# Performance work log

Hardware: AMD Instinct MI355X
Metric: run time of the kernel (lower is better)

## Reference

```python
import jax, jax.numpy as jnp
import jax.scipy.linalg as jsl
import numpy as np

EPS = 1e-6          # config.eps
MIN_EIG = 1e-4      # config.min_eigenvalue
B, N, K = 2, 2048, 3


def _so3_generators():
    # standard so(3) basis: [G_c]_{kl} = -eps_{ckl}
    G = np.zeros((3, 3, 3), np.float32)
    G[0, 1, 2] = -1.0; G[0, 2, 1] = 1.0
    G[1, 0, 2] = 1.0;  G[1, 2, 0] = -1.0
    G[2, 0, 1] = -1.0; G[2, 1, 0] = 1.0
    return jnp.asarray(G)


def _spd(key, b, n, k):
    # well-conditioned SPD covariances (as a real model would produce)
    A = jax.random.normal(key, (b, n, k, k), jnp.float32)
    return jnp.einsum('bnkl,bnml->bnkm', A, A) / k + 0.5 * jnp.eye(k, dtype=jnp.float32)


def setup_inputs() -> dict:
    key = jax.random.key(0)
    k0, k1, k2, k3 = jax.random.split(key, 4)
    Sigma_prior = _spd(k0, B, N, K)
    Sigma_q = _spd(k1, B, N, K)
    phi = jax.random.normal(k2, (B, N, K), jnp.float32)          # gauge field, C == K == 3
    beta = jax.random.uniform(k3, (B, N, N), jnp.float32) / N    # attention-like weights, rows O(1)
    return {
        'Sigma_prior': Sigma_prior,
        'Sigma_q': Sigma_q,
        'phi': phi,
        'beta': beta,
        'generators': _so3_generators(),
    }


def _batched_expm(mats):
    # mats: (B, N, K, K) -> elementwise matrix exponential
    b, n, k, _ = mats.shape
    return jax.vmap(jsl.expm)(mats.reshape(-1, k, k)).reshape(b, n, k, k)


def reference(Sigma_prior, Sigma_q, phi, beta, generators):
    b, n, k, _ = Sigma_prior.shape
    I = jnp.eye(k, dtype=Sigma_prior.dtype)

    # precisions (regularized inverses)
    Lambda_p = jnp.linalg.inv(Sigma_prior + EPS * I)   # (B,N,K,K)
    Lambda_q = jnp.linalg.inv(Sigma_q + EPS * I)       # (B,N,K,K)

    # gauge transport Omega_ij = e^{phi_i} e^{-phi_j}
    phi_mat = jnp.einsum('bnc,ckl->bnkl', phi, generators)
    exp_phi = _batched_expm(phi_mat)
    exp_neg_phi = _batched_expm(-phi_mat)
    Omega = jnp.einsum('bikl,bjlm->bijkm', exp_phi, exp_neg_phi)   # (B,N,N,K,K)

    # transported neighbor precision: Omega Lambda_q Omega^T
    Lt = jnp.einsum('bijkl,bjlm,bijnm->bijkn', Omega, Lambda_q, Omega)

    # incoming social term: sum_j beta_ij * Lt_ij
    M_in = jnp.einsum('bij,bijkl->bikl', beta, Lt)

    # outgoing recoil: (sum_j beta_ji) * Lambda_q_i
    M_out = beta.sum(axis=1)[..., None, None] * Lambda_q

    M = Lambda_p + M_in + M_out
    M = 0.5 * (M + jnp.swapaxes(M, -1, -2))

    # eigenvalue floor + inverse via eigh
    w, V = jnp.linalg.eigh(M)
    w = jnp.maximum(w, MIN_EIG)
    M_pd = jnp.einsum('bnkl,bnl,bnml->bnkm', V, w, V)
    M_inv = jnp.einsum('bnkl,bnl,bnml->bnkm', V, 1.0 / w, V)
    return M_pd, M_inv
```

## Files before the change

kernel.cpp:

```cpp
#include <hip/hip_runtime.h>
#include <math.h>

#define EPS_REG 1e-6f
#define MIN_EIG_F 1e-4f
#define RB 8
#define NCH2 32


__device__ __forceinline__ void sym_inv3(const float m[3][3], float o[3][3]) {
    float c00 = m[1][1]*m[2][2] - m[1][2]*m[2][1];
    float c01 = m[1][2]*m[2][0] - m[1][0]*m[2][2];
    float c02 = m[1][0]*m[2][1] - m[1][1]*m[2][0];
    float det = m[0][0]*c00 + m[0][1]*c01 + m[0][2]*c02;
    float inv = 1.0f / det;
    o[0][0] = c00*inv;
    o[1][0] = c01*inv;
    o[2][0] = c02*inv;
    o[0][1] = (m[0][2]*m[2][1]-m[0][1]*m[2][2])*inv;
    o[1][1] = (m[0][0]*m[2][2]-m[0][2]*m[2][0])*inv;
    o[2][1] = (m[0][1]*m[2][0]-m[0][0]*m[2][1])*inv;
    o[0][2] = (m[0][1]*m[1][2]-m[0][2]*m[1][1])*inv;
    o[1][2] = (m[0][2]*m[1][0]-m[0][0]*m[1][2])*inv;
    o[2][2] = (m[0][0]*m[1][1]-m[0][1]*m[1][0])*inv;
}

__device__ __forceinline__ void jrot(float A[3][3], float V[3][3], int p, int q) {
    float apq = A[p][q];
    if (fabsf(apq) < 1e-20f) return;
    float theta = (A[q][q] - A[p][p]) / (2.0f * apq);
    float t = 1.0f / (fabsf(theta) + sqrtf(1.0f + theta*theta));
    if (theta < 0.0f) t = -t;
    float c = 1.0f / sqrtf(1.0f + t*t);
    float s = t * c;
    int r = 3 - p - q;
    float apq_t = t*apq;
    A[p][p] -= apq_t;
    A[q][q] += apq_t;
    A[p][q] = 0.0f; A[q][p] = 0.0f;
    float arp = A[r][p], arq = A[r][q];
    A[r][p] = c*arp - s*arq; A[p][r] = A[r][p];
    A[r][q] = s*arp + c*arq; A[q][r] = A[r][q];
    #pragma unroll
    for (int k = 0; k < 3; k++) {
        float vkp = V[k][p], vkq = V[k][q];
        V[k][p] = c*vkp - s*vkq;
        V[k][q] = s*vkp + c*vkq;
    }
}

__global__ void precompute_kernel(const float* __restrict__ Sp,
                                  const float* __restrict__ Sq,
                                  const float* __restrict__ phi,
                                  float* __restrict__ Lp,
                                  float* __restrict__ Lq,
                                  float* __restrict__ Rm,
                                  float* __restrict__ S,
                                  int BN) {
    int t = blockIdx.x * blockDim.x + threadIdx.x;
    if (t >= BN) return;

    float m[3][3], lq[3][3], lp[3][3];
    const float* p = Sq + (size_t)t * 9;
    #pragma unroll
    for (int i = 0; i < 3; i++)
        #pragma unroll
        for (int j = 0; j < 3; j++) m[i][j] = p[i*3 + j];
    m[0][0] += EPS_REG; m[1][1] += EPS_REG; m[2][2] += EPS_REG;
    sym_inv3(m, lq);

    p = Sp + (size_t)t * 9;
    #pragma unroll
    for (int i = 0; i < 3; i++)
        #pragma unroll
        for (int j = 0; j < 3; j++) m[i][j] = p[i*3 + j];
    m[0][0] += EPS_REG; m[1][1] += EPS_REG; m[2][2] += EPS_REG;
    sym_inv3(m, lp);

    float* o = Lq + (size_t)t * 6;
    o[0]=lq[0][0]; o[1]=lq[0][1]; o[2]=lq[0][2]; o[3]=lq[1][1]; o[4]=lq[1][2]; o[5]=lq[2][2];
    o = Lp + (size_t)t * 6;
    o[0]=lp[0][0]; o[1]=lp[0][1]; o[2]=lp[0][2]; o[3]=lp[1][1]; o[4]=lp[1][2]; o[5]=lp[2][2];

    float w0 = phi[(size_t)t*3], w1 = phi[(size_t)t*3+1], w2 = phi[(size_t)t*3+2];
    float th2 = w0*w0 + w1*w1 + w2*w2;
    float th = sqrtf(th2);
    float a, b;
    if (th < 1e-4f) { a = 1.0f - th2*(1.0f/6.0f); b = 0.5f - th2*(1.0f/24.0f); }
    else            { a = sinf(th)/th;            b = (1.0f - cosf(th))/th2; }
    float R[3][3];
    R[0][0] = 1.0f + b*(w0*w0 - th2); R[0][1] = -a*w2 + b*w0*w1;        R[0][2] =  a*w1 + b*w0*w2;
    R[1][0] =  a*w2 + b*w0*w1;        R[1][1] = 1.0f + b*(w1*w1 - th2); R[1][2] = -a*w0 + b*w1*w2;
    R[2][0] = -a*w1 + b*w0*w2;        R[2][1] =  a*w0 + b*w1*w2;        R[2][2] = 1.0f + b*(w2*w2 - th2);
    o = Rm + (size_t)t * 9;
    #pragma unroll
    for (int i = 0; i < 3; i++)
        #pragma unroll
        for (int j = 0; j < 3; j++) o[i*3 + j] = R[i][j];

    float U[3][3], Sv[3][3];
    #pragma unroll
    for (int i = 0; i < 3; i++)
        #pragma unroll
        for (int j = 0; j < 3; j++)
            U[i][j] = lq[i][0]*R[0][j] + lq[i][1]*R[1][j] + lq[i][2]*R[2][j];
    #pragma unroll
    for (int i = 0; i < 3; i++)
        #pragma unroll
        for (int j = 0; j < 3; j++)
            Sv[i][j] = R[0][i]*U[0][j] + R[1][i]*U[1][j] + R[2][i]*U[2][j];
    o = S + (size_t)t * 6;
    o[0]=Sv[0][0]; o[1]=Sv[0][1]; o[2]=Sv[0][2]; o[3]=Sv[1][1]; o[4]=Sv[1][2]; o[5]=Sv[2][2];
}

__global__ __launch_bounds__(256) void fused_beta_kernel(
        const float* __restrict__ beta,
        const float* __restrict__ S,
        float* __restrict__ T,
        float* __restrict__ partial,
        int B, int N) {
    int tid = threadIdx.x;
    int grow0 = blockIdx.x * RB;
    int b = grow0 / N;
    int chunksPerB = N / RB;
    int chunk = (grow0 - b * N) / RB;
    const float* sb = S + (size_t)b * N * 6;

    float acc[RB][6];
    #pragma unroll
    for (int r = 0; r < RB; r++)
        #pragma unroll
        for (int c = 0; c < 6; c++) acc[r][c] = 0.0f;

    int jtiles = N / 1024;
    for (int jt = 0; jt < jtiles; jt++) {
        int c0 = jt * 1024 + 4 * tid;
        float4 s4[6];
        const float4* sp = (const float4*)(sb + (size_t)c0 * 6);
        #pragma unroll
        for (int u = 0; u < 6; u++) s4[u] = sp[u];
        const float* sv = (const float*)s4;

        float csum0 = 0.f, csum1 = 0.f, csum2 = 0.f, csum3 = 0.f;
        #pragma unroll
        for (int r = 0; r < RB; r++) {
            float4 w4 = *(const float4*)(beta + (size_t)(grow0 + r) * N + c0);
            csum0 += w4.x; csum1 += w4.y; csum2 += w4.z; csum3 += w4.w;
            #pragma unroll
            for (int c = 0; c < 6; c++) {
                acc[r][c] += w4.x * sv[0*6 + c];
                acc[r][c] += w4.y * sv[1*6 + c];
                acc[r][c] += w4.z * sv[2*6 + c];
                acc[r][c] += w4.w * sv[3*6 + c];
            }
        }
        *(float4*)(partial + ((size_t)b * chunksPerB + chunk) * N + c0) =
            make_float4(csum0, csum1, csum2, csum3);
    }

    __shared__ float red[256][49];
    __shared__ float red2[4][48];
    #pragma unroll
    for (int r = 0; r < RB; r++)
        #pragma unroll
        for (int c = 0; c < 6; c++)
            red[tid][r * 6 + c] = acc[r][c];
    __syncthreads();
    if (tid < 192) {
        int v = tid % 48, grp = tid / 48;
        float s = 0.0f;
        #pragma unroll 8
        for (int r = 0; r < 64; r++) s += red[grp * 64 + r][v];
        red2[grp][v] = s;
    }
    __syncthreads();
    if (tid < 48) {
        float v = red2[0][tid] + red2[1][tid] + red2[2][tid] + red2[3][tid];
        T[(size_t)grow0 * 6 + tid] = v;
    }
}

__global__ void colsum_hop_kernel(const float* __restrict__ partial,
                                  float* __restrict__ partial2,
                                  int B, int N) {
    int colTiles = N / 256;
    int idx = blockIdx.x;
    int ct  = idx % colTiles;
    int g   = (idx / colTiles) % NCH2;
    int b   = idx / (colTiles * NCH2);
    int col = ct * 256 + threadIdx.x;
    int chunksPerB = N / RB;
    int chg = chunksPerB / NCH2;
    const float* p = partial + ((size_t)b * chunksPerB + g * chg) * N + col;
    float s = 0.0f;
    #pragma unroll 8
    for (int k = 0; k < chg; k++) { s += *p; p += N; }
    partial2[((size_t)b * NCH2 + g) * N + col] = s;
}

__global__ void finalize_kernel(const float* __restrict__ Lp,
                                const float* __restrict__ Lq,
                                const float* __restrict__ Rm,
                                const float* __restrict__ T,
                                const float* __restrict__ partial2,
                                float* __restrict__ out,
                                int B, int N) {
    int t = blockIdx.x * blockDim.x + threadIdx.x;
    int BN = B * N;
    if (t >= BN) return;
    int b = t / N;
    int i = t - b * N;

    float cs = 0.0f;
    #pragma unroll 8
    for (int c = 0; c < NCH2; c++)
        cs += partial2[((size_t)b * NCH2 + c) * N + i];

    const float* p = Rm + (size_t)t * 9;
    float R[3][3];
    #pragma unroll
    for (int ii = 0; ii < 3; ii++)
        #pragma unroll
        for (int jj = 0; jj < 3; jj++) R[ii][jj] = p[ii*3 + jj];

    const float* tp = T + (size_t)t * 6;
    float Tm[3][3] = {{tp[0],tp[1],tp[2]},{tp[1],tp[3],tp[4]},{tp[2],tp[4],tp[5]}};
    const float* lpp = Lp + (size_t)t * 6;
    const float* lqp = Lq + (size_t)t * 6;
    float Lpf[3][3] = {{lpp[0],lpp[1],lpp[2]},{lpp[1],lpp[3],lpp[4]},{lpp[2],lpp[4],lpp[5]}};
    float Lqf[3][3] = {{lqp[0],lqp[1],lqp[2]},{lqp[1],lqp[3],lqp[4]},{lqp[2],lqp[4],lqp[5]}};

    float U[3][3], M[3][3];
    #pragma unroll
    for (int ii = 0; ii < 3; ii++)
        #pragma unroll
        for (int jj = 0; jj < 3; jj++)
            U[ii][jj] = R[ii][0]*Tm[0][jj] + R[ii][1]*Tm[1][jj] + R[ii][2]*Tm[2][jj];
    #pragma unroll
    for (int ii = 0; ii < 3; ii++)
        #pragma unroll
        for (int jj = 0; jj < 3; jj++) {
            float min_ij = U[ii][0]*R[jj][0] + U[ii][1]*R[jj][1] + U[ii][2]*R[jj][2];
            M[ii][jj] = Lpf[ii][jj] + min_ij + cs * Lqf[ii][jj];
        }
    float A[3][3];
    #pragma unroll
    for (int ii = 0; ii < 3; ii++)
        #pragma unroll
        for (int jj = 0; jj < 3; jj++) A[ii][jj] = 0.5f * (M[ii][jj] + M[jj][ii]);

    float V[3][3] = {{1,0,0},{0,1,0},{0,0,1}};
    #pragma unroll
    for (int sweep = 0; sweep < 6; sweep++) {
        jrot(A, V, 0, 1);
        jrot(A, V, 0, 2);
        jrot(A, V, 1, 2);
    }
    float w0 = fmaxf(A[0][0], MIN_EIG_F);
    float w1 = fmaxf(A[1][1], MIN_EIG_F);
    float w2 = fmaxf(A[2][2], MIN_EIG_F);
    float iw0 = 1.0f/w0, iw1 = 1.0f/w1, iw2 = 1.0f/w2;

    float* opd = out + (size_t)t * 9;
    float* oin = out + (size_t)BN * 9 + (size_t)t * 9;
    #pragma unroll
    for (int ii = 0; ii < 3; ii++)
        #pragma unroll
        for (int jj = 0; jj < 3; jj++) {
            float pd = V[ii][0]*w0*V[jj][0] + V[ii][1]*w1*V[jj][1] + V[ii][2]*w2*V[jj][2];
            float iv = V[ii][0]*iw0*V[jj][0] + V[ii][1]*iw1*V[jj][1] + V[ii][2]*iw2*V[jj][2];
            opd[ii*3 + jj] = pd;
            oin[ii*3 + jj] = iv;
        }
}

extern "C" void kernel_launch(void* const* d_in, const int* in_sizes, int n_in,
                              void* d_out, int out_size, void* d_ws, size_t ws_size,
                              hipStream_t stream) {
    const float* Sp   = (const float*)d_in[0];
    const float* Sq   = (const float*)d_in[1];
    const float* phi  = (const float*)d_in[2];
    const float* beta = (const float*)d_in[3];

    int BN = in_sizes[2] / 3;
    int N  = (int)((long long)in_sizes[3] / BN);
    int B  = BN / N;

    float* ws = (float*)d_ws;
    float* Lp = ws;
    float* Lq = Lp + (size_t)BN * 6;
    float* Rm = Lq + (size_t)BN * 6;
    float* S  = Rm + (size_t)BN * 9;
    float* T  = S  + (size_t)BN * 6;
    float* partial  = T + (size_t)BN * 6;
    float* partial2 = partial + (size_t)BN / RB * N;

    float* outf = (float*)d_out;

    precompute_kernel<<<(BN + 63)/64, 64, 0, stream>>>(Sp, Sq, phi, Lp, Lq, Rm, S, BN);

    fused_beta_kernel<<<BN / RB, 256, 0, stream>>>(beta, S, T, partial, B, N);

    int colTiles = N / 256;
    colsum_hop_kernel<<<B * NCH2 * colTiles, 256, 0, stream>>>(partial, partial2, B, N);

    finalize_kernel<<<(BN + 63)/64, 64, 0, stream>>>(Lp, Lq, Rm, T, partial2, outf, B, N);
}
```

Measured before the change: 26.84 us.

## Fuse column-sum reduction into finalize and recompute precisions instead of storing

Removes the separate colsum_hop kernel. The finalize kernel now reduces the partial column sums directly with 4 sub-waves per 64 points. Lp, Lq and the rotation matrices are no longer written to workspace; finalize recomputes them from the raw inputs. Global loads and stores in the precompute and finalize kernels are staged through shared memory with coalesced float4 accesses. This saves one launch and intermediate traffic, at the cost of a longer serial column reduction per block and only 64 of 256 threads doing the math.

```diff
diff --git a/kernel.cpp b/kernel.cpp
--- a/kernel.cpp
+++ b/kernel.cpp
@@ -4,7 +4,6 @@
 #define EPS_REG 1e-6f
 #define MIN_EIG_F 1e-4f
 #define RB 8
-#define NCH2 32
 
 
 __device__ __forceinline__ void sym_inv3(const float m[3][3], float o[3][3]) {
@@ -22,6 +21,17 @@
     o[0][2] = (m[0][1]*m[1][2]-m[0][2]*m[1][1])*inv;
     o[1][2] = (m[0][2]*m[1][0]-m[0][0]*m[1][2])*inv;
     o[2][2] = (m[0][0]*m[1][1]-m[0][1]*m[1][0])*inv;
+}
+
+__device__ __forceinline__ void rodrigues(float w0, float w1, float w2, float R[3][3]) {
+    float th2 = w0*w0 + w1*w1 + w2*w2;
+    float th = sqrtf(th2);
+    float a, b;
+    if (th < 1e-4f) { a = 1.0f - th2*(1.0f/6.0f); b = 0.5f - th2*(1.0f/24.0f); }
+    else            { a = sinf(th)/th;            b = (1.0f - cosf(th))/th2; }
+    R[0][0] = 1.0f + b*(w0*w0 - th2); R[0][1] = -a*w2 + b*w0*w1;        R[0][2] =  a*w1 + b*w0*w2;
+    R[1][0] =  a*w2 + b*w0*w1;        R[1][1] = 1.0f + b*(w1*w1 - th2); R[1][2] = -a*w0 + b*w1*w2;
+    R[2][0] = -a*w1 + b*w0*w2;        R[2][1] =  a*w0 + b*w1*w2;        R[2][2] = 1.0f + b*(w2*w2 - th2);
 }
 
 __device__ __forceinline__ void jrot(float A[3][3], float V[3][3], int p, int q) {
@@ -48,68 +58,53 @@
     }
 }
 
-__global__ void precompute_kernel(const float* __restrict__ Sp,
-                                  const float* __restrict__ Sq,
-                                  const float* __restrict__ phi,
-                                  float* __restrict__ Lp,
-                                  float* __restrict__ Lq,
-                                  float* __restrict__ Rm,
-                                  float* __restrict__ S,
-                                  int BN) {
-    int t = blockIdx.x * blockDim.x + threadIdx.x;
-    if (t >= BN) return;
-
-    float m[3][3], lq[3][3], lp[3][3];
-    const float* p = Sq + (size_t)t * 9;
+__global__ __launch_bounds__(64) void precompute_S_kernel(
+        const float* __restrict__ Sq,
+        const float* __restrict__ phi,
+        float* __restrict__ S,
+        int BN) {
+    __shared__ float sq_s[576];
+    __shared__ float ph_s[192];
+    __shared__ float so_s[384];
+    int tid = threadIdx.x;
+    int p0 = blockIdx.x * 64;
+
+    const float4* src = (const float4*)(Sq + (size_t)p0 * 9);
+    #pragma unroll
+    for (int i = tid; i < 144; i += 64) ((float4*)sq_s)[i] = src[i];
+    const float4* psrc = (const float4*)(phi + (size_t)p0 * 3);
+    if (tid < 48) ((float4*)ph_s)[tid] = psrc[tid];
+    __syncthreads();
+
+    float m[3][3], lq[3][3];
     #pragma unroll
     for (int i = 0; i < 3; i++)
         #pragma unroll
-        for (int j = 0; j < 3; j++) m[i][j] = p[i*3 + j];
+        for (int j = 0; j < 3; j++) m[i][j] = sq_s[tid*9 + i*3 + j];
     m[0][0] += EPS_REG; m[1][1] += EPS_REG; m[2][2] += EPS_REG;
     sym_inv3(m, lq);
 
-    p = Sp + (size_t)t * 9;
-    #pragma unroll
-    for (int i = 0; i < 3; i++)
-        #pragma unroll
-        for (int j = 0; j < 3; j++) m[i][j] = p[i*3 + j];
-    m[0][0] += EPS_REG; m[1][1] += EPS_REG; m[2][2] += EPS_REG;
-    sym_inv3(m, lp);
-
-    float* o = Lq + (size_t)t * 6;
-    o[0]=lq[0][0]; o[1]=lq[0][1]; o[2]=lq[0][2]; o[3]=lq[1][1]; o[4]=lq[1][2]; o[5]=lq[2][2];
-    o = Lp + (size_t)t * 6;
-    o[0]=lp[0][0]; o[1]=lp[0][1]; o[2]=lp[0][2]; o[3]=lp[1][1]; o[4]=lp[1][2]; o[5]=lp[2][2];
-
-    float w0 = phi[(size_t)t*3], w1 = phi[(size_t)t*3+1], w2 = phi[(size_t)t*3+2];
-    float th2 = w0*w0 + w1*w1 + w2*w2;
-    float th = sqrtf(th2);
-    float a, b;
-    if (th < 1e-4f) { a = 1.0f - th2*(1.0f/6.0f); b = 0.5f - th2*(1.0f/24.0f); }
-    else            { a = sinf(th)/th;            b = (1.0f - cosf(th))/th2; }
     float R[3][3];
-    R[0][0] = 1.0f + b*(w0*w0 - th2); R[0][1] = -a*w2 + b*w0*w1;        R[0][2] =  a*w1 + b*w0*w2;
-    R[1][0] =  a*w2 + b*w0*w1;        R[1][1] = 1.0f + b*(w1*w1 - th2); R[1][2] = -a*w0 + b*w1*w2;
-    R[2][0] = -a*w1 + b*w0*w2;        R[2][1] =  a*w0 + b*w1*w2;        R[2][2] = 1.0f + b*(w2*w2 - th2);
-    o = Rm + (size_t)t * 9;
-    #pragma unroll
-    for (int i = 0; i < 3; i++)
-        #pragma unroll
-        for (int j = 0; j < 3; j++) o[i*3 + j] = R[i][j];
-
-    float U[3][3], Sv[3][3];
+    rodrigues(ph_s[tid*3], ph_s[tid*3+1], ph_s[tid*3+2], R);
+
+    float U[3][3];
     #pragma unroll
     for (int i = 0; i < 3; i++)
         #pragma unroll
         for (int j = 0; j < 3; j++)
             U[i][j] = lq[i][0]*R[0][j] + lq[i][1]*R[1][j] + lq[i][2]*R[2][j];
-    #pragma unroll
-    for (int i = 0; i < 3; i++)
-        #pragma unroll
-        for (int j = 0; j < 3; j++)
-            Sv[i][j] = R[0][i]*U[0][j] + R[1][i]*U[1][j] + R[2][i]*U[2][j];
-    o = S + (size_t)t * 6;
-    o[0]=Sv[0][0]; o[1]=Sv[0][1]; o[2]=Sv[0][2]; o[3]=Sv[1][1]; o[4]=Sv[1][2]; o[5]=Sv[2][2];
+    float s00 = R[0][0]*U[0][0] + R[1][0]*U[1][0] + R[2][0]*U[2][0];
+    float s01 = R[0][0]*U[0][1] + R[1][0]*U[1][1] + R[2][0]*U[2][1];
+    float s02 = R[0][0]*U[0][2] + R[1][0]*U[1][2] + R[2][0]*U[2][2];
+    float s11 = R[0][1]*U[0][1] + R[1][1]*U[1][1] + R[2][1]*U[2][1];
+    float s12 = R[0][1]*U[0][2] + R[1][1]*U[1][2] + R[2][1]*U[2][2];
+    float s22 = R[0][2]*U[0][2] + R[1][2]*U[1][2] + R[2][2]*U[2][2];
+    so_s[tid*6+0]=s00; so_s[tid*6+1]=s01; so_s[tid*6+2]=s02;
+    so_s[tid*6+3]=s11; so_s[tid*6+4]=s12; so_s[tid*6+5]=s22;
+    __syncthreads();
+    float4* dst = (float4*)(S + (size_t)p0 * 6);
+    #pragma unroll
+    for (int i = tid; i < 96; i += 64) dst[i] = ((float4*)so_s)[i];
 }
 
 __global__ __launch_bounds__(256) void fused_beta_kernel(
@@ -179,98 +174,112 @@
     }
 }
 
-__global__ void colsum_hop_kernel(const float* __restrict__ partial,
-                                  float* __restrict__ partial2,
-                                  int B, int N) {
-    int colTiles = N / 256;
-    int idx = blockIdx.x;
-    int ct  = idx % colTiles;
-    int g   = (idx / colTiles) % NCH2;
-    int b   = idx / (colTiles * NCH2);
-    int col = ct * 256 + threadIdx.x;
-    int chunksPerB = N / RB;
-    int chg = chunksPerB / NCH2;
-    const float* p = partial + ((size_t)b * chunksPerB + g * chg) * N + col;
-    float s = 0.0f;
+__global__ __launch_bounds__(256) void finalize_kernel(
+        const float* __restrict__ Sp,
+        const float* __restrict__ Sq,
+        const float* __restrict__ phi,
+        const float* __restrict__ T,
+        const float* __restrict__ partial,
+        float* __restrict__ out,
+        int B, int N) {
+    int tid  = threadIdx.x;
+    int lane = tid & 63;
+    int sub  = tid >> 6;
+    int p0   = blockIdx.x * 64;
+    int BN   = B * N;
+    int b    = p0 / N;
+    int i0   = p0 - b * N;
+    int chunks = N / RB;
+
+    __shared__ float redc[4][64];
+    __shared__ float sp_s[576], sq_s[576], ph_s[192], t_s[384];
+    __shared__ float o1_s[576], o2_s[576];
+
+    int cpg = chunks / 4;
+    float csp = 0.0f;
+    const float* pp = partial + ((size_t)b * chunks + sub * cpg) * N + (i0 + lane);
     #pragma unroll 8
-    for (int k = 0; k < chg; k++) { s += *p; p += N; }
-    partial2[((size_t)b * NCH2 + g) * N + col] = s;
-}
-
-__global__ void finalize_kernel(const float* __restrict__ Lp,
-                                const float* __restrict__ Lq,
-                                const float* __restrict__ Rm,
-                                const float* __restrict__ T,
-                                const float* __restrict__ partial2,
-                                float* __restrict__ out,
-                                int B, int N) {
-    int t = blockIdx.x * blockDim.x + threadIdx.x;
-    int BN = B * N;
-    if (t >= BN) return;
-    int b = t / N;
-    int i = t - b * N;
-
-    float cs = 0.0f;
-    #pragma unroll 8
-    for (int c = 0; c < NCH2; c++)
-        cs += partial2[((size_t)b * NCH2 + c) * N + i];
-
-    const float* p = Rm + (size_t)t * 9;
-    float R[3][3];
-    #pragma unroll
-    for (int ii = 0; ii < 3; ii++)
-        #pragma unroll
-        for (int jj = 0; jj < 3; jj++) R[ii][jj] = p[ii*3 + jj];
-
-    const float* tp = T + (size_t)t * 6;
-    float Tm[3][3] = {{tp[0],tp[1],tp[2]},{tp[1],tp[3],tp[4]},{tp[2],tp[4],tp[5]}};
-    const float* lpp = Lp + (size_t)t * 6;
-    const float* lqp = Lq + (size_t)t * 6;
-    float Lpf[3][3] = {{lpp[0],lpp[1],lpp[2]},{lpp[1],lpp[3],lpp[4]},{lpp[2],lpp[4],lpp[5]}};
-    float Lqf[3][3] = {{lqp[0],lqp[1],lqp[2]},{lqp[1],lqp[3],lqp[4]},{lqp[2],lqp[4],lqp[5]}};
-
-    float U[3][3], M[3][3];
-    #pragma unroll
-    for (int ii = 0; ii < 3; ii++)
-        #pragma unroll
-        for (int jj = 0; jj < 3; jj++)
-            U[ii][jj] = R[ii][0]*Tm[0][jj] + R[ii][1]*Tm[1][jj] + R[ii][2]*Tm[2][jj];
-    #pragma unroll
-    for (int ii = 0; ii < 3; ii++)
-        #pragma unroll
-        for (int jj = 0; jj < 3; jj++) {
-            float min_ij = U[ii][0]*R[jj][0] + U[ii][1]*R[jj][1] + U[ii][2]*R[jj][2];
-            M[ii][jj] = Lpf[ii][jj] + min_ij + cs * Lqf[ii][jj];
+    for (int c = 0; c < cpg; c++) { csp += *pp; pp += (size_t)N; }
+    redc[sub][lane] = csp;
+
+    {
+        const float4* s1 = (const float4*)(Sp + (size_t)p0 * 9);
+        const float4* s2 = (const float4*)(Sq + (size_t)p0 * 9);
+        if (tid < 144) { ((float4*)sp_s)[tid] = s1[tid]; ((float4*)sq_s)[tid] = s2[tid]; }
+        const float4* s3 = (const float4*)(phi + (size_t)p0 * 3);
+        if (tid < 48) ((float4*)ph_s)[tid] = s3[tid];
+        const float4* s4 = (const float4*)(T + (size_t)p0 * 6);
+        if (tid < 96) ((float4*)t_s)[tid] = s4[tid];
+    }
+    __syncthreads();
+
+    if (tid < 64) {
+        float cs = redc[0][lane] + redc[1][lane] + redc[2][lane] + redc[3][lane];
+
+        float m[3][3], lp[3][3], lq[3][3];
+        #pragma unroll
+        for (int i = 0; i < 3; i++)
+            #pragma unroll
+            for (int j = 0; j < 3; j++) m[i][j] = sq_s[lane*9 + i*3 + j];
+        m[0][0] += EPS_REG; m[1][1] += EPS_REG; m[2][2] += EPS_REG;
+        sym_inv3(m, lq);
+        #pragma unroll
+        for (int i = 0; i < 3; i++)
+            #pragma unroll
+            for (int j = 0; j < 3; j++) m[i][j] = sp_s[lane*9 + i*3 + j];
+        m[0][0] += EPS_REG; m[1][1] += EPS_REG; m[2][2] += EPS_REG;
+        sym_inv3(m, lp);
+
+        float R[3][3];
+        rodrigues(ph_s[lane*3], ph_s[lane*3+1], ph_s[lane*3+2], R);
+
+        const float* tp = t_s + lane * 6;
+        float Tm[3][3] = {{tp[0],tp[1],tp[2]},{tp[1],tp[3],tp[4]},{tp[2],tp[4],tp[5]}};
+
+        float U[3][3], M[3][3];
+        #pragma unroll
+        for (int ii = 0; ii < 3; ii++)
+            #pragma unroll
+            for (int jj = 0; jj < 3; jj++)
+                U[ii][jj] = R[ii][0]*Tm[0][jj] + R[ii][1]*Tm[1][jj] + R[ii][2]*Tm[2][jj];
+        #pragma unroll
+        for (int ii = 0; ii < 3; ii++)
+            #pragma unroll
+            for (int jj = 0; jj < 3; jj++) {
+                float min_ij = U[ii][0]*R[jj][0] + U[ii][1]*R[jj][1] + U[ii][2]*R[jj][2];
+                M[ii][jj] = lp[ii][jj] + min_ij + cs * lq[ii][jj];
+            }
+        float A[3][3];
+        #pragma unroll
+        for (int ii = 0; ii < 3; ii++)
+            #pragma unroll
+            for (int jj = 0; jj < 3; jj++) A[ii][jj] = 0.5f * (M[ii][jj] + M[jj][ii]);
+
+        float V[3][3] = {{1,0,0},{0,1,0},{0,0,1}};
+        #pragma unroll
+        for (int sweep = 0; sweep < 6; sweep++) {
+            jrot(A, V, 0, 1);
+            jrot(A, V, 0, 2);
+            jrot(A, V, 1, 2);
         }
-    float A[3][3];
-    #pragma unroll
-    for (int ii = 0; ii < 3; ii++)
-        #pragma unroll
-        for (int jj = 0; jj < 3; jj++) A[ii][jj] = 0.5f * (M[ii][jj] + M[jj][ii]);
-
-    float V[3][3] = {{1,0,0},{0,1,0},{0,0,1}};
-    #pragma unroll
-    for (int sweep = 0; sweep < 6; sweep++) {
-        jrot(A, V, 0, 1);
-        jrot(A, V, 0, 2);
-        jrot(A, V, 1, 2);
-    }
-    float w0 = fmaxf(A[0][0], MIN_EIG_F);
-    float w1 = fmaxf(A[1][1], MIN_EIG_F);
-    float w2 = fmaxf(A[2][2], MIN_EIG_F);
-    float iw0 = 1.0f/w0, iw1 = 1.0f/w1, iw2 = 1.0f/w2;
-
-    float* opd = out + (size_t)t * 9;
-    float* oin = out + (size_t)BN * 9 + (size_t)t * 9;
-    #pragma unroll
-    for (int ii = 0; ii < 3; ii++)
-        #pragma unroll
-        for (int jj = 0; jj < 3; jj++) {
-            float pd = V[ii][0]*w0*V[jj][0] + V[ii][1]*w1*V[jj][1] + V[ii][2]*w2*V[jj][2];
-            float iv = V[ii][0]*iw0*V[jj][0] + V[ii][1]*iw1*V[jj][1] + V[ii][2]*iw2*V[jj][2];
-            opd[ii*3 + jj] = pd;
-            oin[ii*3 + jj] = iv;
-        }
+        float w0 = fmaxf(A[0][0], MIN_EIG_F);
+        float w1 = fmaxf(A[1][1], MIN_EIG_F);
+        float w2 = fmaxf(A[2][2], MIN_EIG_F);
+        float iw0 = 1.0f/w0, iw1 = 1.0f/w1, iw2 = 1.0f/w2;
+
+        #pragma unroll
+        for (int ii = 0; ii < 3; ii++)
+            #pragma unroll
+            for (int jj = 0; jj < 3; jj++) {
+                o1_s[lane*9 + ii*3 + jj] = V[ii][0]*w0*V[jj][0] + V[ii][1]*w1*V[jj][1] + V[ii][2]*w2*V[jj][2];
+                o2_s[lane*9 + ii*3 + jj] = V[ii][0]*iw0*V[jj][0] + V[ii][1]*iw1*V[jj][1] + V[ii][2]*iw2*V[jj][2];
+            }
+    }
+    __syncthreads();
+
+    float4* d1 = (float4*)(out + (size_t)p0 * 9);
+    float4* d2 = (float4*)(out + (size_t)BN * 9 + (size_t)p0 * 9);
+    if (tid < 144) { d1[tid] = ((float4*)o1_s)[tid]; d2[tid] = ((float4*)o2_s)[tid]; }
 }
 
 extern "C" void kernel_launch(void* const* d_in, const int* in_sizes, int n_in,
@@ -286,22 +295,15 @@
     int B  = BN / N;
 
     float* ws = (float*)d_ws;
-    float* Lp = ws;
-    float* Lq = Lp + (size_t)BN * 6;
-    float* Rm = Lq + (size_t)BN * 6;
-    float* S  = Rm + (size_t)BN * 9;
-    float* T  = S  + (size_t)BN * 6;
-    float* partial  = T + (size_t)BN * 6;
-    float* partial2 = partial + (size_t)BN / RB * N;
+    float* S  = ws;
+    float* T  = S + (size_t)BN * 6;
+    float* partial = T + (size_t)BN * 6;
 
     float* outf = (float*)d_out;
 
-    precompute_kernel<<<(BN + 63)/64, 64, 0, stream>>>(Sp, Sq, phi, Lp, Lq, Rm, S, BN);
+    precompute_S_kernel<<<BN / 64, 64, 0, stream>>>(Sq, phi, S, BN);
 
     fused_beta_kernel<<<BN / RB, 256, 0, stream>>>(beta, S, T, partial, B, N);
 
-    int colTiles = N / 256;
-    colsum_hop_kernel<<<B * NCH2 * colTiles, 256, 0, stream>>>(partial, partial2, B, N);
-
-    finalize_kernel<<<(BN + 63)/64, 64, 0, stream>>>(Lp, Lq, Rm, T, partial2, outf, B, N);
-}
+    finalize_kernel<<<BN / 64, 256, 0, stream>>>(Sp, Sq, phi, T, partial, outf, B, N);
+}
```

Result: no change. 26.95 us (+0.4%).
